# Performance work log

Hardware: AMD Instinct MI355X
Metric: run time of the kernel (lower is better)

The kernel has to match this reference:

```python
import jax, jax.numpy as jnp
import numpy as np

SEQ_LENS = [1024, 768, 512, 896, 640, 384, 1024, 896]
TOTAL = sum(SEQ_LENS)  # 6144
EMBED = 768
NUM_HEADS = 12
HEAD_DIM = EMBED // NUM_HEADS
FFN = 3072
LN_EPS = 1e-5


def _pad_maps():
    # static (numpy) index maps for ragged <-> padded layout
    B, S = len(SEQ_LENS), max(SEQ_LENS)
    offs = np.cumsum([0] + SEQ_LENS)
    pad_idx = np.zeros((B, S), np.int32)
    valid = np.zeros((B, S), bool)
    for i, L in enumerate(SEQ_LENS):
        pad_idx[i, :L] = np.arange(offs[i], offs[i] + L)
        valid[i, :L] = True
    flat_b = np.concatenate([np.full(L, i, np.int32) for i, L in enumerate(SEQ_LENS)])
    flat_p = np.concatenate([np.arange(L, dtype=np.int32) for L in SEQ_LENS])
    return jnp.asarray(pad_idx), jnp.asarray(valid), jnp.asarray(flat_b), jnp.asarray(flat_p)

PAD_IDX, VALID, FLAT_B, FLAT_P = _pad_maps()


def _layernorm(x, g, b):
    mu = jnp.mean(x, axis=-1, keepdims=True)
    var = jnp.mean(jnp.square(x - mu), axis=-1, keepdims=True)
    return (x - mu) * jax.lax.rsqrt(var + LN_EPS) * g + b


def setup_inputs() -> dict:
    key = jax.random.key(0)
    ks = jax.random.split(key, 8)
    return {
        "hidden_states": jax.random.normal(ks[0], (TOTAL, EMBED), jnp.float32),
        "attention_mask": jnp.ones((TOTAL,), jnp.int32),
        "in_proj_w": 0.02 * jax.random.normal(ks[1], (3 * EMBED, EMBED), jnp.float32),
        "in_proj_b": jnp.zeros((3 * EMBED,), jnp.float32),
        "out_proj_w": 0.02 * jax.random.normal(ks[2], (EMBED, EMBED), jnp.float32),
        "out_proj_b": jnp.zeros((EMBED,), jnp.float32),
        "ln1_g": jnp.ones((EMBED,), jnp.float32),
        "ln1_b": jnp.zeros((EMBED,), jnp.float32),
        "fc1_w": 0.02 * jax.random.normal(ks[3], (FFN, EMBED), jnp.float32),
        "fc1_b": jnp.zeros((FFN,), jnp.float32),
        "fc2_w": 0.02 * jax.random.normal(ks[4], (EMBED, FFN), jnp.float32),
        "fc2_b": jnp.zeros((EMBED,), jnp.float32),
        "ln2_g": jnp.ones((EMBED,), jnp.float32),
        "ln2_b": jnp.zeros((EMBED,), jnp.float32),
    }


def reference(hidden_states, attention_mask, in_proj_w, in_proj_b, out_proj_w,
              out_proj_b, ln1_g, ln1_b, fc1_w, fc1_b, fc2_w, fc2_b, ln2_g, ln2_b):
    B, S = PAD_IDX.shape
    residual = hidden_states
    x = _layernorm(hidden_states, ln1_g, ln1_b)  # pre-LN (do_layer_norm_before)

    # ragged -> padded [B, S, E]; key validity combines padding mask and ragged tail
    xp = x[PAD_IDX]
    key_valid = VALID & (attention_mask[PAD_IDX] != 0)

    # fused QKV projection (nn.MultiheadAttention in_proj)
    qkv = xp @ in_proj_w.T + in_proj_b  # [B, S, 3E]
    q, k, v = jnp.split(qkv, 3, axis=-1)
    q = q.reshape(B, S, NUM_HEADS, HEAD_DIM) * (1.0 / np.sqrt(HEAD_DIM))
    k = k.reshape(B, S, NUM_HEADS, HEAD_DIM)
    v = v.reshape(B, S, NUM_HEADS, HEAD_DIM)

    scores = jnp.einsum('bqhd,bkhd->bhqk', q, k)  # [B, H, S, S]
    causal = jnp.tril(jnp.ones((S, S), bool))
    mask = causal[None, None] & key_valid[:, None, None, :]
    scores = jnp.where(mask, scores, jnp.float32(-1e30))
    probs = jax.nn.softmax(scores, axis=-1)
    ctx = jnp.einsum('bhqk,bkhd->bqhd', probs, v).reshape(B, S, EMBED)
    attn = ctx @ out_proj_w.T + out_proj_b

    # padded -> ragged, residual
    h = residual + attn[FLAT_B, FLAT_P]

    # FFN block (pre-LN)
    residual = h
    h = _layernorm(h, ln2_g, ln2_b)
    h = jax.nn.relu(h @ fc1_w.T + fc1_b)
    h = h @ fc2_w.T + fc2_b
    return residual + h
```

## Files before the change

kernel.cpp:

```cpp
#include <hip/hip_runtime.h>
#include <hip/hip_bf16.h>

#define TOTAL 6144
#define EMBED 768
#define QKV3  2304
#define FFN   3072
#define NH    12
#define HD    64

typedef unsigned short u16;
typedef unsigned int u32;
typedef float f32x4 __attribute__((ext_vector_type(4)));
typedef __bf16 bf16x8 __attribute__((ext_vector_type(8)));

__device__ __constant__ int BOFF[9] = {0, 1024, 1792, 2304, 3200, 3840, 4224, 5248, 6144};

__device__ __forceinline__ u16 f2b(float f) {
    __bf16 h = (__bf16)f;
    return __builtin_bit_cast(u16, h);
}

__device__ __forceinline__ void gload_lds16(const u16* g, u16* l) {
    __builtin_amdgcn_global_load_lds(
        (const __attribute__((address_space(1))) u32*)(uintptr_t)g,
        (__attribute__((address_space(3))) u32*)(uintptr_t)l, 16, 0, 0);
}

__device__ __forceinline__ float rowmax16(float x) {
    int v;
    v = __builtin_amdgcn_mov_dpp(__float_as_int(x), 0xB1, 0xF, 0xF, true);
    x = fmaxf(x, __int_as_float(v));
    v = __builtin_amdgcn_mov_dpp(__float_as_int(x), 0x4E, 0xF, 0xF, true);
    x = fmaxf(x, __int_as_float(v));
    v = __builtin_amdgcn_mov_dpp(__float_as_int(x), 0x124, 0xF, 0xF, true);
    x = fmaxf(x, __int_as_float(v));
    v = __builtin_amdgcn_mov_dpp(__float_as_int(x), 0x128, 0xF, 0xF, true);
    x = fmaxf(x, __int_as_float(v));
    return x;
}

__global__ void cvt4_kernel(const float* __restrict__ s0, u16* __restrict__ d0, int n0,
                            const float* __restrict__ s1, u16* __restrict__ d1, int n1,
                            const float* __restrict__ s2, u16* __restrict__ d2, int n2,
                            const float* __restrict__ s3, u16* __restrict__ d3, int n3) {
    int i = blockIdx.x * blockDim.x + threadIdx.x;
    const float* s;
    u16* d;
    int j = i;
    if (j < n0) { s = s0; d = d0; }
    else {
        j -= n0;
        if (j < n1) { s = s1; d = d1; }
        else {
            j -= n1;
            if (j < n2) { s = s2; d = d2; }
            else {
                j -= n2;
                if (j >= n3) return;
                s = s3; d = d3;
            }
        }
    }
    float4 v = ((const float4*)s)[j];
    ushort4 o;
    o.x = f2b(v.x); o.y = f2b(v.y); o.z = f2b(v.z); o.w = f2b(v.w);
    ((ushort4*)d)[j] = o;
}

__global__ void maskbits_kernel(const int* __restrict__ am, u32* __restrict__ mb) {
    int i = blockIdx.x * 64 + threadIdx.x;
    unsigned long long bal = __ballot(am[i] != 0);
    if (threadIdx.x == 0) {
        mb[blockIdx.x * 2] = (u32)bal;
        mb[blockIdx.x * 2 + 1] = (u32)(bal >> 32);
    }
}

__global__ __launch_bounds__(256) void ln_kernel(const float* __restrict__ x,
                                                 const float* __restrict__ g,
                                                 const float* __restrict__ b,
                                                 u16* __restrict__ out) {
    int row = blockIdx.x * 4 + (threadIdx.x >> 6);
    int lane = threadIdx.x & 63;
    const float* xr = x + (size_t)row * EMBED;
    float4 v[3];
    float s = 0.f, sq = 0.f;
#pragma unroll
    for (int c = 0; c < 3; ++c) {
        v[c] = *(const float4*)(xr + c * 256 + lane * 4);
        s += v[c].x + v[c].y + v[c].z + v[c].w;
        sq += v[c].x * v[c].x + v[c].y * v[c].y + v[c].z * v[c].z + v[c].w * v[c].w;
    }
#pragma unroll
    for (int o = 32; o; o >>= 1) {
        s += __shfl_xor(s, o);
        sq += __shfl_xor(sq, o);
    }
    float mu = s * (1.f / 768.f);
    float var = sq * (1.f / 768.f) - mu * mu;
    float rs = rsqrtf(var + 1e-5f);
    u16* orow = out + (size_t)row * EMBED;
#pragma unroll
    for (int c = 0; c < 3; ++c) {
        int col = c * 256 + lane * 4;
        float4 gg = *(const float4*)(g + col);
        float4 bb = *(const float4*)(b + col);
        ushort4 o;
        o.x = f2b((v[c].x - mu) * rs * gg.x + bb.x);
        o.y = f2b((v[c].y - mu) * rs * gg.y + bb.y);
        o.z = f2b((v[c].z - mu) * rs * gg.z + bb.z);
        o.w = f2b((v[c].w - mu) * rs * gg.w + bb.w);
        *(ushort4*)(orow + col) = o;
    }
}

template <int RELU, int RES, int OUTB, int OUTF, int VTR>
__global__ __launch_bounds__(256) void gemm128(const u16* __restrict__ A,
                                               const u16* __restrict__ B,
                                               const float* __restrict__ bias,
                                               const float* __restrict__ res,
                                               u16* __restrict__ outb,
                                               float* __restrict__ outf,
                                               u16* __restrict__ vout,
                                               int M, int N, int K) {
    __shared__ u16 As[2][128][64];
    __shared__ u16 Bs[2][128][64];
    int t = threadIdx.x;
    int lane = t & 63, w = t >> 6;
    int wr = w >> 1, wc = w & 1;
    int gx = gridDim.x;
    int nwg = gx * gridDim.y;
    int flat = blockIdx.y * gx + blockIdx.x;
    int swz = (flat & 7) * (nwg >> 3) + (flat >> 3);
    int m0 = (swz / gx) * 128, n0 = (swz % gx) * 128;
    int lr = lane >> 3;
    int lcg = (lane & 7) ^ (lr & 7);
    int c16 = lane & 15, hi = lane >> 4;

    f32x4 acc[4][4];
#pragma unroll
    for (int m = 0; m < 4; ++m)
#pragma unroll
        for (int n = 0; n < 4; ++n) acc[m][n] = (f32x4)0.f;

    const u16* Ab = A + (size_t)(m0 + w * 32 + lr) * K + lcg * 8;
    const u16* Bb = B + (size_t)(n0 + w * 32 + lr) * K + lcg * 8;

    int nk = K >> 6;
#pragma unroll
    for (int i = 0; i < 4; ++i) {
        gload_lds16(Ab + (size_t)(i * 8) * K, &As[0][w * 32 + i * 8][0]);
        gload_lds16(Bb + (size_t)(i * 8) * K, &Bs[0][w * 32 + i * 8][0]);
    }

    for (int tk = 0; tk < nk; ++tk) {
        int cur = tk & 1;
        if (tk + 1 < nk) {
            int k1 = (tk + 1) << 6;
#pragma unroll
            for (int i = 0; i < 4; ++i) {
                gload_lds16(Ab + (size_t)(i * 8) * K + k1, &As[cur ^ 1][w * 32 + i * 8][0]);
                gload_lds16(Bb + (size_t)(i * 8) * K + k1, &Bs[cur ^ 1][w * 32 + i * 8][0]);
            }
            asm volatile("s_waitcnt vmcnt(8)" ::: "memory");
        } else {
            asm volatile("s_waitcnt vmcnt(0)" ::: "memory");
        }
        __builtin_amdgcn_sched_barrier(0);
        __builtin_amdgcn_s_barrier();
#pragma unroll
        for (int ks = 0; ks < 2; ++ks) {
            bf16x8 af[4], bfr[4];
#pragma unroll
            for (int m = 0; m < 4; ++m)
                af[m] = *(const bf16x8*)&As[cur][wr * 64 + m * 16 + c16][((ks * 4 + hi) ^ (c16 & 7)) * 8];
#pragma unroll
            for (int n = 0; n < 4; ++n)
                bfr[n] = *(const bf16x8*)&Bs[cur][wc * 64 + n * 16 + c16][((ks * 4 + hi) ^ (c16 & 7)) * 8];
#pragma unroll
            for (int m = 0; m < 4; ++m)
#pragma unroll
                for (int n = 0; n < 4; ++n)
                    acc[m][n] = __builtin_amdgcn_mfma_f32_16x16x32_bf16(af[m], bfr[n], acc[m][n], 0, 0, 0);
        }
        asm volatile("s_waitcnt lgkmcnt(0)" ::: "memory");
        __builtin_amdgcn_sched_barrier(0);
        __builtin_amdgcn_s_barrier();
    }

#pragma unroll
    for (int m = 0; m < 4; ++m)
#pragma unroll
        for (int n = 0; n < 4; ++n) {
            int cg = n0 + wc * 64 + n * 16 + c16;
            float bv = bias[cg];
            float vj[4];
#pragma unroll
            for (int j = 0; j < 4; ++j) {
                int rg = m0 + wr * 64 + m * 16 + hi * 4 + j;
                float v = acc[m][n][j] + bv;
                if (RELU) v = fmaxf(v, 0.f);
                if (RES) v += res[(size_t)rg * N + cg];
                vj[j] = v;
                if (OUTB) outb[(size_t)rg * N + cg] = f2b(v);
                if (OUTF) outf[(size_t)rg * N + cg] = v;
            }
            if (VTR && cg >= 2 * EMBED) {
                ushort4 tv;
                tv.x = f2b(vj[0]); tv.y = f2b(vj[1]); tv.z = f2b(vj[2]); tv.w = f2b(vj[3]);
                int rgb = m0 + wr * 64 + m * 16 + hi * 4;
                *(ushort4*)&vout[(size_t)(cg - 2 * EMBED) * TOTAL + rgb] = tv;
            }
        }
}

__global__ __launch_bounds__(64, 2) void attn_mfma(const u16* __restrict__ qkv,
                                                   const u16* __restrict__ vT,
                                                   const u32* __restrict__ mbits,
                                                   u16* __restrict__ ctx) {
    __shared__ u16 Pl[32][64];
    int l = threadIdx.x;
    int hi = l >> 4, c = l & 15;
    int bid = blockIdx.x;
    int swz = (bid & 7) * 288 + (bid >> 3);
    int h = swz / 192;
    int qt = 191 - (swz % 192);
    int r0 = qt * 32;
    int b = 0;
#pragma unroll
    for (int i = 0; i < 8; ++i)
        if (r0 >= BOFF[i + 1]) b = i + 1;
    int boff = BOFF[b];
    int p0 = r0 - boff;
    int nchunks = (p0 >> 6) + 1;
    int nfull = (p0 >= 63) ? (((p0 - 63) >> 6) + 1) : 0;
    const float SCALE = 0.125f * 1.44269504f;

    bf16x8 qa[2][2];
#pragma unroll
    for (int m = 0; m < 2; ++m)
#pragma unroll
        for (int ks = 0; ks < 2; ++ks)
            qa[m][ks] = *(const bf16x8*)&qkv[(size_t)(r0 + m * 16 + c) * QKV3 + h * HD + ks * 32 + hi * 8];

    bf16x8 vones;
#pragma unroll
    for (int j = 0; j < 8; ++j) vones[j] = (__bf16)1.0f;

    f32x4 oacc[2][4], lacc[2];
    float mrun[2][4];
#pragma unroll
    for (int m = 0; m < 2; ++m) {
        lacc[m] = (f32x4)0.f;
#pragma unroll
        for (int nt = 0; nt < 4; ++nt) oacc[m][nt] = (f32x4)0.f;
#pragma unroll
        for (int r = 0; r < 4; ++r) mrun[m][r] = -1e30f;
    }

    for (int kc = 0; kc < nchunks; ++kc) {
        int k0 = kc << 6;
        bf16x8 kb[2][4], vb[2][4];
#pragma unroll
        for (int ks = 0; ks < 2; ++ks)
#pragma unroll
            for (int nt = 0; nt < 4; ++nt) {
                kb[ks][nt] = *(const bf16x8*)&qkv[(size_t)(boff + k0 + nt * 16 + c) * QKV3 +
                                                  EMBED + h * HD + ks * 32 + hi * 8];
                vb[ks][nt] = *(const bf16x8*)&vT[(size_t)(h * HD + nt * 16 + c) * TOTAL +
                                                 boff + k0 + ks * 32 + hi * 8];
            }
        int wi = (boff + k0) >> 5;
        u32 mw0 = mbits[wi], mw1 = mbits[wi + 1];

        f32x4 sacc[2][4];
#pragma unroll
        for (int m = 0; m < 2; ++m)
#pragma unroll
            for (int nt = 0; nt < 4; ++nt) sacc[m][nt] = (f32x4)0.f;
#pragma unroll
        for (int ks = 0; ks < 2; ++ks)
#pragma unroll
            for (int m = 0; m < 2; ++m)
#pragma unroll
                for (int nt = 0; nt < 4; ++nt)
                    sacc[m][nt] = __builtin_amdgcn_mfma_f32_16x16x32_bf16(qa[m][ks], kb[ks][nt], sacc[m][nt], 0, 0, 0);

        bool fullmask = ((mw0 & mw1) == 0xFFFFFFFFu);
        if (kc >= nfull) {
#pragma unroll
            for (int m = 0; m < 2; ++m)
#pragma unroll
                for (int nt = 0; nt < 4; ++nt) {
                    int kpos = k0 + nt * 16 + c;
                    u32 mwv = (nt & 2) ? mw1 : mw0;
                    float madd = fullmask ? 0.f
                        : (((mwv >> (((nt & 1) << 4) + c)) & 1u) ? 0.f : -1e30f);
#pragma unroll
                    for (int r = 0; r < 4; ++r) {
                        int qp = p0 + m * 16 + 4 * hi + r;
                        sacc[m][nt][r] = (kpos <= qp) ? (sacc[m][nt][r] + madd) : -1e30f;
                    }
                }
        } else if (!fullmask) {
#pragma unroll
            for (int m = 0; m < 2; ++m)
#pragma unroll
                for (int nt = 0; nt < 4; ++nt) {
                    u32 mwv = (nt & 2) ? mw1 : mw0;
                    float madd = ((mwv >> (((nt & 1) << 4) + c)) & 1u) ? 0.f : -1e30f;
#pragma unroll
                    for (int r = 0; r < 4; ++r) sacc[m][nt][r] += madd;
                }
        }

        float mx[2][4];
        int small = 1;
#pragma unroll
        for (int m = 0; m < 2; ++m)
#pragma unroll
            for (int r = 0; r < 4; ++r) {
                float v = fmaxf(fmaxf(sacc[m][0][r], sacc[m][1][r]),
                                fmaxf(sacc[m][2][r], sacc[m][3][r]));
                v = rowmax16(v);
                mx[m][r] = v;
                small &= (v <= mrun[m][r]) ? 1 : 0;
            }
        if (!__all(small)) {
#pragma unroll
            for (int m = 0; m < 2; ++m)
#pragma unroll
                for (int r = 0; r < 4; ++r) {
                    float mn = fmaxf(mrun[m][r], mx[m][r]);
                    float f = exp2f((mrun[m][r] - mn) * SCALE);
                    mrun[m][r] = mn;
                    lacc[m][r] *= f;
#pragma unroll
                    for (int nt = 0; nt < 4; ++nt) oacc[m][nt][r] *= f;
                }
        }

        float negm[2][4];
#pragma unroll
        for (int m = 0; m < 2; ++m)
#pragma unroll
            for (int r = 0; r < 4; ++r) negm[m][r] = -mrun[m][r] * SCALE;
#pragma unroll
        for (int m = 0; m < 2; ++m)
#pragma unroll
            for (int nt = 0; nt < 4; ++nt)
#pragma unroll
                for (int r = 0; r < 4; ++r) {
                    float p = exp2f(fmaf(sacc[m][nt][r], SCALE, negm[m][r]));
                    int row = m * 16 + 4 * hi + r;
                    int cch = ((nt * 2 + (c >> 3)) ^ (row & 7)) << 3;
                    Pl[row][cch + (c & 7)] = f2b(p);
                }

#pragma unroll
        for (int ks = 0; ks < 2; ++ks) {
            bf16x8 pa[2];
#pragma unroll
            for (int m = 0; m < 2; ++m)
                pa[m] = *(const bf16x8*)&Pl[m * 16 + c][(((ks * 4 + hi) ^ (c & 7)) << 3)];
#pragma unroll
            for (int m = 0; m < 2; ++m) {
                lacc[m] = __builtin_amdgcn_mfma_f32_16x16x32_bf16(pa[m], vones, lacc[m], 0, 0, 0);
#pragma unroll
                for (int nt = 0; nt < 4; ++nt)
                    oacc[m][nt] = __builtin_amdgcn_mfma_f32_16x16x32_bf16(pa[m], vb[ks][nt], oacc[m][nt], 0, 0, 0);
            }
        }
    }

#pragma unroll
    for (int m = 0; m < 2; ++m)
#pragma unroll
        for (int r = 0; r < 4; ++r) {
            float inv = 1.0f / lacc[m][r];
#pragma unroll
            for (int nt = 0; nt < 4; ++nt)
                ctx[(size_t)(r0 + m * 16 + 4 * hi + r) * EMBED + h * HD + nt * 16 + c] =
                    f2b(oacc[m][nt][r] * inv);
        }
}

extern "C" void kernel_launch(void* const* d_in, const int* in_sizes, int n_in,
                              void* d_out, int out_size, void* d_ws, size_t ws_size,
                              hipStream_t stream) {
    (void)in_sizes; (void)n_in; (void)out_size; (void)ws_size;
    const float* hidden = (const float*)d_in[0];
    const int*   amask  = (const int*)d_in[1];
    const float* in_w   = (const float*)d_in[2];
    const float* in_b   = (const float*)d_in[3];
    const float* out_w  = (const float*)d_in[4];
    const float* out_b  = (const float*)d_in[5];
    const float* ln1g   = (const float*)d_in[6];
    const float* ln1b   = (const float*)d_in[7];
    const float* fc1w   = (const float*)d_in[8];
    const float* fc1b   = (const float*)d_in[9];
    const float* fc2w   = (const float*)d_in[10];
    const float* fc2b   = (const float*)d_in[11];
    const float* ln2g   = (const float*)d_in[12];
    const float* ln2b   = (const float*)d_in[13];
    float* out = (float*)d_out;

    char* ws = (char*)d_ws;
    size_t off = 0;
    auto alloc = [&](size_t bytes) {
        void* p = ws + off;
        off += (bytes + 255) & ~(size_t)255;
        return p;
    };
    u16* w_in_bf  = (u16*)alloc((size_t)QKV3 * EMBED * 2);
    u16* w_out_bf = (u16*)alloc((size_t)EMBED * EMBED * 2);
    u16* w_fc1_bf = (u16*)alloc((size_t)FFN * EMBED * 2);
    u16* w_fc2_bf = (u16*)alloc((size_t)EMBED * FFN * 2);
    u16* xln  = (u16*)alloc((size_t)TOTAL * EMBED * 2);
    u16* qkv  = (u16*)alloc((size_t)TOTAL * QKV3 * 2);
    u16* ctx  = (u16*)alloc((size_t)TOTAL * EMBED * 2);
    float* hmid = (float*)alloc((size_t)TOTAL * EMBED * 4);
    u16* hln  = (u16*)alloc((size_t)TOTAL * EMBED * 2);
    u16* f1o  = (u16*)alloc((size_t)TOTAL * FFN * 2);
    u32* mbits = (u32*)alloc(192 * 4);
    u16* vT = hln;

    cvt4_kernel<<<6912, 256, 0, stream>>>(in_w, w_in_bf, 442368,
                                          out_w, w_out_bf, 147456,
                                          fc1w, w_fc1_bf, 589824,
                                          fc2w, w_fc2_bf, 589824);
    maskbits_kernel<<<96, 64, 0, stream>>>(amask, mbits);

    ln_kernel<<<TOTAL / 4, 256, 0, stream>>>(hidden, ln1g, ln1b, xln);
    gemm128<0, 0, 1, 0, 1><<<dim3(QKV3 / 128, TOTAL / 128), 256, 0, stream>>>(
        xln, w_in_bf, in_b, nullptr, qkv, nullptr, vT, TOTAL, QKV3, EMBED);
    attn_mfma<<<dim3((TOTAL / 32) * NH), 64, 0, stream>>>(qkv, vT, mbits, ctx);
    gemm128<0, 1, 0, 1, 0><<<dim3(EMBED / 128, TOTAL / 128), 256, 0, stream>>>(
        ctx, w_out_bf, out_b, hidden, nullptr, hmid, nullptr, TOTAL, EMBED, EMBED);
    ln_kernel<<<TOTAL / 4, 256, 0, stream>>>(hmid, ln2g, ln2b, hln);
    gemm128<1, 0, 1, 0, 0><<<dim3(FFN / 128, TOTAL / 128), 256, 0, stream>>>(
        hln, w_fc1_bf, fc1b, nullptr, f1o, nullptr, nullptr, TOTAL, FFN, EMBED);
    gemm128<0, 1, 0, 1, 0><<<dim3(EMBED / 128, TOTAL / 128), 256, 0, stream>>>(
        f1o, w_fc2_bf, fc2b, hmid, nullptr, out, nullptr, TOTAL, EMBED, FFN);
}
```

Measured before the change: 221.8 us.

## Split attention KV chunks across four waves with LDS split-softmax combine

The attention kernel now launches 256 threads per query tile. Each of its four waves handles every fourth 64-key chunk, and the partial outputs, running maxima and sums are merged through a shared-memory union using flash-decoding style rescaling. This shortens the serial KV loop per block, which is long for late query tiles, at the cost of an LDS combine, two barriers and higher per-block resource use. Separately, the mask-bit ballot kernel is folded into the weight conversion kernel as extra blocks to save one launch.

```diff
diff --git a/kernel.cpp b/kernel.cpp
--- a/kernel.cpp
+++ b/kernel.cpp
@@ -39,10 +39,21 @@
     return x;
 }
 
-__global__ void cvt4_kernel(const float* __restrict__ s0, u16* __restrict__ d0, int n0,
-                            const float* __restrict__ s1, u16* __restrict__ d1, int n1,
-                            const float* __restrict__ s2, u16* __restrict__ d2, int n2,
-                            const float* __restrict__ s3, u16* __restrict__ d3, int n3) {
+__global__ void cvt4m_kernel(const float* __restrict__ s0, u16* __restrict__ d0, int n0,
+                             const float* __restrict__ s1, u16* __restrict__ d1, int n1,
+                             const float* __restrict__ s2, u16* __restrict__ d2, int n2,
+                             const float* __restrict__ s3, u16* __restrict__ d3, int n3,
+                             const int* __restrict__ am, u32* __restrict__ mb) {
+    if (blockIdx.x >= 6912) {
+        int g = (blockIdx.x - 6912) * 4 + (threadIdx.x >> 6);
+        int lane = threadIdx.x & 63;
+        unsigned long long bal = __ballot(am[g * 64 + lane] != 0);
+        if (lane == 0) {
+            mb[g * 2] = (u32)bal;
+            mb[g * 2 + 1] = (u32)(bal >> 32);
+        }
+        return;
+    }
     int i = blockIdx.x * blockDim.x + threadIdx.x;
     const float* s;
     u16* d;
@@ -65,15 +76,6 @@
     ushort4 o;
     o.x = f2b(v.x); o.y = f2b(v.y); o.z = f2b(v.z); o.w = f2b(v.w);
     ((ushort4*)d)[j] = o;
-}
-
-__global__ void maskbits_kernel(const int* __restrict__ am, u32* __restrict__ mb) {
-    int i = blockIdx.x * 64 + threadIdx.x;
-    unsigned long long bal = __ballot(am[i] != 0);
-    if (threadIdx.x == 0) {
-        mb[blockIdx.x * 2] = (u32)bal;
-        mb[blockIdx.x * 2 + 1] = (u32)(bal >> 32);
-    }
 }
 
 __global__ __launch_bounds__(256) void ln_kernel(const float* __restrict__ x,
@@ -214,12 +216,21 @@
         }
 }
 
-__global__ __launch_bounds__(64, 2) void attn_mfma(const u16* __restrict__ qkv,
-                                                   const u16* __restrict__ vT,
-                                                   const u32* __restrict__ mbits,
-                                                   u16* __restrict__ ctx) {
-    __shared__ u16 Pl[32][64];
-    int l = threadIdx.x;
+struct CombineBufs {
+    float om[4][64][33];
+    float ml[4][32][2];
+};
+union AttnLds {
+    u16 pl[4][32][64];
+    CombineBufs c;
+};
+
+__global__ __launch_bounds__(256, 4) void attn_mfma(const u16* __restrict__ qkv,
+                                                    const u16* __restrict__ vT,
+                                                    const u32* __restrict__ mbits,
+                                                    u16* __restrict__ ctx) {
+    __shared__ AttnLds S;
+    int t = threadIdx.x, l = t & 63, w = t >> 6;
     int hi = l >> 4, c = l & 15;
     int bid = blockIdx.x;
     int swz = (bid & 7) * 288 + (bid >> 3);
@@ -258,7 +269,7 @@
         for (int r = 0; r < 4; ++r) mrun[m][r] = -1e30f;
     }
 
-    for (int kc = 0; kc < nchunks; ++kc) {
+    for (int kc = w; kc < nchunks; kc += 4) {
         int k0 = kc << 6;
         bf16x8 kb[2][4], vb[2][4];
 #pragma unroll
@@ -354,7 +365,7 @@
                     float p = exp2f(fmaf(sacc[m][nt][r], SCALE, negm[m][r]));
                     int row = m * 16 + 4 * hi + r;
                     int cch = ((nt * 2 + (c >> 3)) ^ (row & 7)) << 3;
-                    Pl[row][cch + (c & 7)] = f2b(p);
+                    S.pl[w][row][cch + (c & 7)] = f2b(p);
                 }
 
 #pragma unroll
@@ -362,7 +373,7 @@
             bf16x8 pa[2];
 #pragma unroll
             for (int m = 0; m < 2; ++m)
-                pa[m] = *(const bf16x8*)&Pl[m * 16 + c][(((ks * 4 + hi) ^ (c & 7)) << 3)];
+                pa[m] = *(const bf16x8*)&S.pl[w][m * 16 + c][(((ks * 4 + hi) ^ (c & 7)) << 3)];
 #pragma unroll
             for (int m = 0; m < 2; ++m) {
                 lacc[m] = __builtin_amdgcn_mfma_f32_16x16x32_bf16(pa[m], vones, lacc[m], 0, 0, 0);
@@ -373,16 +384,52 @@
         }
     }
 
+    __syncthreads();
 #pragma unroll
     for (int m = 0; m < 2; ++m)
 #pragma unroll
+        for (int nt = 0; nt < 4; ++nt)
+            *(f32x4*)&S.c.om[w][nt * 16 + c][m * 16 + 4 * hi] = oacc[m][nt];
+    if (c == 0) {
+#pragma unroll
+        for (int m = 0; m < 2; ++m)
+#pragma unroll
+            for (int r = 0; r < 4; ++r) {
+                int row = m * 16 + 4 * hi + r;
+                S.c.ml[w][row][0] = mrun[m][r];
+                S.c.ml[w][row][1] = lacc[m][r];
+            }
+    }
+    __syncthreads();
+
+#pragma unroll
+    for (int m = 0; m < 2; ++m) {
+        int rbase = m * 16 + 4 * hi;
+        float Mm[4], ll[4];
+#pragma unroll
         for (int r = 0; r < 4; ++r) {
-            float inv = 1.0f / lacc[m][r];
-#pragma unroll
-            for (int nt = 0; nt < 4; ++nt)
-                ctx[(size_t)(r0 + m * 16 + 4 * hi + r) * EMBED + h * HD + nt * 16 + c] =
-                    f2b(oacc[m][nt][r] * inv);
-        }
+            float mm = -1e30f;
+#pragma unroll
+            for (int wv = 0; wv < 4; ++wv) mm = fmaxf(mm, S.c.ml[wv][rbase + r][0]);
+            Mm[r] = mm;
+            float lt = 0.f;
+#pragma unroll
+            for (int wv = 0; wv < 4; ++wv)
+                lt += exp2f((S.c.ml[wv][rbase + r][0] - mm) * SCALE) * S.c.ml[wv][rbase + r][1];
+            ll[r] = lt;
+        }
+        f32x4 o = (f32x4)0.f;
+#pragma unroll
+        for (int wv = 0; wv < 4; ++wv) {
+            f32x4 ov = *(const f32x4*)&S.c.om[wv][w * 16 + c][rbase];
+#pragma unroll
+            for (int r = 0; r < 4; ++r)
+                o[r] += exp2f((S.c.ml[wv][rbase + r][0] - Mm[r]) * SCALE) * ov[r];
+        }
+#pragma unroll
+        for (int r = 0; r < 4; ++r)
+            ctx[(size_t)(r0 + rbase + r) * EMBED + h * HD + w * 16 + c] = f2b(o[r] / ll[r]);
+    }
 }
 
 extern "C" void kernel_launch(void* const* d_in, const int* in_sizes, int n_in,
@@ -425,16 +472,16 @@
     u32* mbits = (u32*)alloc(192 * 4);
     u16* vT = hln;
 
-    cvt4_kernel<<<6912, 256, 0, stream>>>(in_w, w_in_bf, 442368,
-                                          out_w, w_out_bf, 147456,
-                                          fc1w, w_fc1_bf, 589824,
-                                          fc2w, w_fc2_bf, 589824);
-    maskbits_kernel<<<96, 64, 0, stream>>>(amask, mbits);
+    cvt4m_kernel<<<6936, 256, 0, stream>>>(in_w, w_in_bf, 442368,
+                                           out_w, w_out_bf, 147456,
+                                           fc1w, w_fc1_bf, 589824,
+                                           fc2w, w_fc2_bf, 589824,
+                                           amask, mbits);
 
     ln_kernel<<<TOTAL / 4, 256, 0, stream>>>(hidden, ln1g, ln1b, xln);
     gemm128<0, 0, 1, 0, 1><<<dim3(QKV3 / 128, TOTAL / 128), 256, 0, stream>>>(
         xln, w_in_bf, in_b, nullptr, qkv, nullptr, vT, TOTAL, QKV3, EMBED);
-    attn_mfma<<<dim3((TOTAL / 32) * NH), 64, 0, stream>>>(qkv, vT, mbits, ctx);
+    attn_mfma<<<dim3((TOTAL / 32) * NH), 256, 0, stream>>>(qkv, vT, mbits, ctx);
     gemm128<0, 1, 0, 1, 0><<<dim3(EMBED / 128, TOTAL / 128), 256, 0, stream>>>(
         ctx, w_out_bf, out_b, hidden, nullptr, hmid, nullptr, TOTAL, EMBED, EMBED);
     ln_kernel<<<TOTAL / 4, 256, 0, stream>>>(hmid, ln2g, ln2b, hln);
```

After: 295.1 us. 1.33x slower.

## Split long attention query tiles across key segments with a combine pass

Applied to the files above, without the earlier changes.

The attention kernel now splits each query tile's key range into segments of up to four 64-key chunks. Each segment runs as its own workgroup and writes a normalized partial output plus its running max and sum to a scratch buffer. A new combine kernel merges these partials with log-sum-exp weights, which is meant to balance the causal load across many more blocks. The mask-bit kernel is also folded into the weight-conversion launch to save one launch, at the cost of an extra kernel and scratch traffic, and partials are stored in bf16.

```diff
diff --git a/kernel.cpp b/kernel.cpp
--- a/kernel.cpp
+++ b/kernel.cpp
@@ -7,6 +7,9 @@
 #define FFN   3072
 #define NH    12
 #define HD    64
+#define NSEG  412
+#define NCQT  128
+#define SLOTB 4608
 
 typedef unsigned short u16;
 typedef unsigned int u32;
@@ -15,9 +18,38 @@
 
 __device__ __constant__ int BOFF[9] = {0, 1024, 1792, 2304, 3200, 3840, 4224, 5248, 6144};
 
+struct SegT {
+    short segstart[193];
+    short qt_of_seg[NSEG];
+    short cqt[NCQT];
+};
+constexpr SegT make_segt() {
+    SegT s{};
+    const int toff[9] = {0, 32, 56, 72, 100, 120, 132, 164, 192};
+    int tot = 0, cc = 0;
+    for (int qt = 0; qt < 192; ++qt) {
+        int b = 0;
+        for (int i = 0; i < 8; ++i)
+            if (qt >= toff[i + 1]) b = i + 1;
+        int t = qt - toff[b];
+        int nch = t / 2 + 1;
+        int ns = (nch + 3) / 4;
+        s.segstart[qt] = (short)tot;
+        for (int j = 0; j < ns; ++j) s.qt_of_seg[tot + j] = (short)qt;
+        tot += ns;
+        if (ns >= 2) s.cqt[cc++] = (short)qt;
+    }
+    s.segstart[192] = (short)tot;
+    return s;
+}
+__device__ __constant__ SegT SEGT = make_segt();
+
 __device__ __forceinline__ u16 f2b(float f) {
     __bf16 h = (__bf16)f;
     return __builtin_bit_cast(u16, h);
+}
+__device__ __forceinline__ float b2f(u16 h) {
+    union { u32 u; float f; } v; v.u = ((u32)h) << 16; return v.f;
 }
 
 __device__ __forceinline__ void gload_lds16(const u16* g, u16* l) {
@@ -39,10 +71,21 @@
     return x;
 }
 
-__global__ void cvt4_kernel(const float* __restrict__ s0, u16* __restrict__ d0, int n0,
-                            const float* __restrict__ s1, u16* __restrict__ d1, int n1,
-                            const float* __restrict__ s2, u16* __restrict__ d2, int n2,
-                            const float* __restrict__ s3, u16* __restrict__ d3, int n3) {
+__global__ void cvt4m_kernel(const float* __restrict__ s0, u16* __restrict__ d0, int n0,
+                             const float* __restrict__ s1, u16* __restrict__ d1, int n1,
+                             const float* __restrict__ s2, u16* __restrict__ d2, int n2,
+                             const float* __restrict__ s3, u16* __restrict__ d3, int n3,
+                             const int* __restrict__ am, u32* __restrict__ mb) {
+    if (blockIdx.x >= 6912) {
+        int g = (blockIdx.x - 6912) * 4 + (threadIdx.x >> 6);
+        int lane = threadIdx.x & 63;
+        unsigned long long bal = __ballot(am[g * 64 + lane] != 0);
+        if (lane == 0) {
+            mb[g * 2] = (u32)bal;
+            mb[g * 2 + 1] = (u32)(bal >> 32);
+        }
+        return;
+    }
     int i = blockIdx.x * blockDim.x + threadIdx.x;
     const float* s;
     u16* d;
@@ -65,15 +108,6 @@
     ushort4 o;
     o.x = f2b(v.x); o.y = f2b(v.y); o.z = f2b(v.z); o.w = f2b(v.w);
     ((ushort4*)d)[j] = o;
-}
-
-__global__ void maskbits_kernel(const int* __restrict__ am, u32* __restrict__ mb) {
-    int i = blockIdx.x * 64 + threadIdx.x;
-    unsigned long long bal = __ballot(am[i] != 0);
-    if (threadIdx.x == 0) {
-        mb[blockIdx.x * 2] = (u32)bal;
-        mb[blockIdx.x * 2 + 1] = (u32)(bal >> 32);
-    }
 }
 
 __global__ __launch_bounds__(256) void ln_kernel(const float* __restrict__ x,
@@ -217,14 +251,18 @@
 __global__ __launch_bounds__(64, 2) void attn_mfma(const u16* __restrict__ qkv,
                                                    const u16* __restrict__ vT,
                                                    const u32* __restrict__ mbits,
-                                                   u16* __restrict__ ctx) {
+                                                   u16* __restrict__ ctx,
+                                                   char* __restrict__ pbuf) {
     __shared__ u16 Pl[32][64];
     int l = threadIdx.x;
     int hi = l >> 4, c = l & 15;
-    int bid = blockIdx.x;
-    int swz = (bid & 7) * 288 + (bid >> 3);
-    int h = swz / 192;
-    int qt = 191 - (swz % 192);
+    int bidg = blockIdx.x;
+    int swz = (bidg & 7) * (NSEG * NH / 8) + (bidg >> 3);
+    int h = swz / NSEG;
+    int sl = swz % NSEG;
+    int qt = SEGT.qt_of_seg[sl];
+    int seg = sl - SEGT.segstart[qt];
+    int nseg = SEGT.segstart[qt + 1] - SEGT.segstart[qt];
     int r0 = qt * 32;
     int b = 0;
 #pragma unroll
@@ -234,6 +272,8 @@
     int p0 = r0 - boff;
     int nchunks = (p0 >> 6) + 1;
     int nfull = (p0 >= 63) ? (((p0 - 63) >> 6) + 1) : 0;
+    int kc0 = seg * 4;
+    int kc1 = min(kc0 + 4, nchunks);
     const float SCALE = 0.125f * 1.44269504f;
 
     bf16x8 qa[2][2];
@@ -258,7 +298,7 @@
         for (int r = 0; r < 4; ++r) mrun[m][r] = -1e30f;
     }
 
-    for (int kc = 0; kc < nchunks; ++kc) {
+    for (int kc = kc0; kc < kc1; ++kc) {
         int k0 = kc << 6;
         bf16x8 kb[2][4], vb[2][4];
 #pragma unroll
@@ -373,16 +413,74 @@
         }
     }
 
-#pragma unroll
-    for (int m = 0; m < 2; ++m)
-#pragma unroll
-        for (int r = 0; r < 4; ++r) {
-            float inv = 1.0f / lacc[m][r];
-#pragma unroll
-            for (int nt = 0; nt < 4; ++nt)
-                ctx[(size_t)(r0 + m * 16 + 4 * hi + r) * EMBED + h * HD + nt * 16 + c] =
-                    f2b(oacc[m][nt][r] * inv);
-        }
+    if (nseg == 1) {
+#pragma unroll
+        for (int m = 0; m < 2; ++m)
+#pragma unroll
+            for (int r = 0; r < 4; ++r) {
+                float inv = 1.0f / lacc[m][r];
+#pragma unroll
+                for (int nt = 0; nt < 4; ++nt)
+                    ctx[(size_t)(r0 + m * 16 + 4 * hi + r) * EMBED + h * HD + nt * 16 + c] =
+                        f2b(oacc[m][nt][r] * inv);
+            }
+    } else {
+        char* base = pbuf + (size_t)(h * NSEG + sl) * SLOTB;
+        u16* Op = (u16*)base;
+        float* mlp = (float*)(base + 4096);
+#pragma unroll
+        for (int m = 0; m < 2; ++m)
+#pragma unroll
+            for (int r = 0; r < 4; ++r) {
+                int row = m * 16 + 4 * hi + r;
+                float inv = 1.0f / lacc[m][r];
+#pragma unroll
+                for (int nt = 0; nt < 4; ++nt)
+                    Op[row * 64 + nt * 16 + c] = f2b(oacc[m][nt][r] * inv);
+                if (c == 0) {
+                    mlp[row * 2] = mrun[m][r];
+                    mlp[row * 2 + 1] = lacc[m][r];
+                }
+            }
+    }
+}
+
+__global__ __launch_bounds__(64) void attn_combine(const char* __restrict__ pbuf,
+                                                   u16* __restrict__ ctx) {
+    int cid = blockIdx.x;
+    int h = cid % NH;
+    int qt = SEGT.cqt[cid / NH];
+    int s0 = SEGT.segstart[qt];
+    int ns = SEGT.segstart[qt + 1] - s0;
+    int d = threadIdx.x;
+    int r0 = qt * 32;
+    const float SCALE = 0.125f * 1.44269504f;
+
+    const char* bases[4];
+#pragma unroll
+    for (int j = 0; j < 4; ++j)
+        bases[j] = pbuf + (size_t)(h * NSEG + s0 + min(j, ns - 1)) * SLOTB;
+
+    for (int r = 0; r < 32; ++r) {
+        float mj[4], lj[4];
+#pragma unroll
+        for (int j = 0; j < 4; ++j) {
+            const float* mlp = (const float*)(bases[j] + 4096);
+            mj[j] = (j < ns) ? mlp[r * 2] : -1e30f;
+            lj[j] = (j < ns) ? mlp[r * 2 + 1] : 0.f;
+        }
+        float M = fmaxf(fmaxf(mj[0], mj[1]), fmaxf(mj[2], mj[3]));
+        float o = 0.f, wsum = 0.f;
+#pragma unroll
+        for (int j = 0; j < 4; ++j) {
+            if (j < ns) {
+                float e = exp2f((mj[j] - M) * SCALE) * lj[j];
+                wsum += e;
+                o += e * b2f(((const u16*)bases[j])[r * 64 + d]);
+            }
+        }
+        ctx[(size_t)(r0 + r) * EMBED + h * HD + d] = f2b(o / wsum);
+    }
 }
 
 extern "C" void kernel_launch(void* const* d_in, const int* in_sizes, int n_in,
@@ -424,17 +522,19 @@
     u16* f1o  = (u16*)alloc((size_t)TOTAL * FFN * 2);
     u32* mbits = (u32*)alloc(192 * 4);
     u16* vT = hln;
-
-    cvt4_kernel<<<6912, 256, 0, stream>>>(in_w, w_in_bf, 442368,
-                                          out_w, w_out_bf, 147456,
-                                          fc1w, w_fc1_bf, 589824,
-                                          fc2w, w_fc2_bf, 589824);
-    maskbits_kernel<<<96, 64, 0, stream>>>(amask, mbits);
+    char* pbuf = (char*)f1o;
+
+    cvt4m_kernel<<<6936, 256, 0, stream>>>(in_w, w_in_bf, 442368,
+                                           out_w, w_out_bf, 147456,
+                                           fc1w, w_fc1_bf, 589824,
+                                           fc2w, w_fc2_bf, 589824,
+                                           amask, mbits);
 
     ln_kernel<<<TOTAL / 4, 256, 0, stream>>>(hidden, ln1g, ln1b, xln);
     gemm128<0, 0, 1, 0, 1><<<dim3(QKV3 / 128, TOTAL / 128), 256, 0, stream>>>(
         xln, w_in_bf, in_b, nullptr, qkv, nullptr, vT, TOTAL, QKV3, EMBED);
-    attn_mfma<<<dim3((TOTAL / 32) * NH), 64, 0, stream>>>(qkv, vT, mbits, ctx);
+    attn_mfma<<<dim3(NSEG * NH), 64, 0, stream>>>(qkv, vT, mbits, ctx, pbuf);
+    attn_combine<<<dim3(NCQT * NH), 64, 0, stream>>>(pbuf, ctx);
     gemm128<0, 1, 0, 1, 0><<<dim3(EMBED / 128, TOTAL / 128), 256, 0, stream>>>(
         ctx, w_out_bf, out_b, hidden, nullptr, hmid, nullptr, TOTAL, EMBED, EMBED);
     ln_kernel<<<TOTAL / 4, 256, 0, stream>>>(hmid, ln2g, ln2b, hln);
```

Result: slower. 256.9 us (+15.8%).
